# Optimization experiments

Hardware: AMD Instinct MI355X
Metric: run time of the kernel (lower is better)

Reference implementation:

```python
import jax, jax.numpy as jnp
import numpy as np

LAM = 0.01        # self.lam
K_POINTS = 256    # max diagram points kept for matching


def _diagram0(img):
    """0-dim sublevel-set cubical persistence of a 2D image (V-construction,
    4-connectivity) via Kruskal-style union-find over value-sorted pixels.
    Returns (births, deaths, valid) each of shape [H*W]; essential class gets
    death = max(img). Pairs with zero persistence are masked out (as gudhi does)."""
    H, W = img.shape
    N = H * W
    v = img.reshape(-1)
    order = jnp.argsort(v)          # stable ascending filtration order
    rank = jnp.argsort(order)       # rank[i] = position of pixel i in filtration
    idx = jnp.arange(N)
    rows, cols = idx // W, idx % W
    nbr = jnp.stack([
        jnp.where(rows > 0, idx - W, -1),
        jnp.where(rows < H - 1, idx + W, -1),
        jnp.where(cols > 0, idx - 1, -1),
        jnp.where(cols < W - 1, idx + 1, -1)], axis=1)  # [N,4]

    def find(parent, i):
        # root chase with path halving
        def cond(c):
            p, j = c
            return p[j] != j
        def body(c):
            p, j = c
            pj = p[j]
            return p.at[j].set(p[pj]), pj
        p, r = jax.lax.while_loop(cond, body, (parent, i))
        return p, r

    def step(t, carry):
        parent, death = carry
        p = order[t]  # pixel entering the filtration
        def merge(k, carry2):
            parent, death = carry2
            q = nbr[p, k]
            active = (q >= 0) & (rank[jnp.maximum(q, 0)] < t)
            qs = jnp.where(active, jnp.maximum(q, 0), p)
            parent, rp = find(parent, p)
            parent, rq = find(parent, qs)
            do = active & (rp != rq)
            older = jnp.where(rank[rp] < rank[rq], rp, rq)   # smaller birth survives
            young = jnp.where(rank[rp] < rank[rq], rq, rp)   # younger component dies at v[p]
            parent = parent.at[young].set(jnp.where(do, older, parent[young]))
            death = death.at[young].set(jnp.where(do, p, death[young]))
            return parent, death
        return jax.lax.fori_loop(0, 4, merge, (parent, death))

    parent, death = jax.lax.fori_loop(
        0, N, step, (jnp.arange(N), jnp.full((N,), -1, jnp.int32)))
    births = v
    deaths = jnp.where(death >= 0, v[jnp.maximum(death, 0)], jnp.max(v))
    valid = (deaths - births) > 0
    return births, deaths, valid


def _wdist(b1, d1, m1, b2, d2, m2):
    """2-Wasserstein distance between diagrams, approximated by matching the
    top-K points of each diagram sorted by persistence; unmatched points are
    projected to the diagonal (cost pers^2/2). Final (sum cost)^(1/2) (p=2)."""
    def topk(b, d, m):
        pers = jnp.where(m, d - b, 0.0)
        pk, ix = jax.lax.top_k(pers, K_POINTS)
        return b[ix], d[ix], pk
    b1k, d1k, p1 = topk(b1, d1, m1)
    b2k, d2k, p2 = topk(b2, d2, m2)
    has1, has2 = p1 > 0, p2 > 0
    match = (b1k - b2k) ** 2 + (d1k - d2k) ** 2
    cost = (jnp.where(has1 & has2, match, 0.0)
            + jnp.where(has1 & ~has2, p1 ** 2 * 0.5, 0.0)
            + jnp.where(~has1 & has2, p2 ** 2 * 0.5, 0.0))
    return jnp.sqrt(jnp.sum(cost) + 1e-12)


def _topo_loss(model_output, labels):
    pred = jax.nn.sigmoid(model_output)[:, 0]   # squeeze(dim=1) -> [B,H,W]
    msk = labels[:, 0]
    mn = pred.min(axis=(1, 2), keepdims=True)
    mx = pred.max(axis=(1, 2), keepdims=True)
    pq = jnp.round((pred - mn) / (mx - mn) * 10.0) / 10.0   # 11-level quantization
    mq = jnp.round(msk * 10.0) / 10.0
    bm, dm, vm = jax.vmap(_diagram0)(mq)   # pi_mask
    bp, dp, vp = jax.vmap(_diagram0)(pq)   # pi_pred
    per_sample = jax.vmap(_wdist)(bm, dm, vm, bp, dp, vp)
    return LAM * jnp.sum(per_sample) / pred.shape[0]


def setup_inputs():
    key = jax.random.key(0)
    k1, k2 = jax.random.split(key)
    model_output = jax.random.normal(k1, (4, 1, 128, 128), jnp.float32)
    labels = jax.random.uniform(k2, (4, 1, 128, 128), jnp.float32)
    return {"model_output": model_output, "labels": labels}


def reference(model_output, labels):
    return _topo_loss(model_output, labels)
```

## Files before the change

### kernel.cpp

```cpp
#include <hip/hip_runtime.h>
#include <stdint.h>

#define NPIX 16384
#define IMW 128
#define NIMG 8
#define NLVL 11
#define BIGK 0xFFFFFFFFu
#define IMASK 16383u
#define DONE 0x0D0E0D0Eu

__device__ __forceinline__ unsigned findk(volatile unsigned* par, unsigned i) {
    unsigned k = par[i];
    for (;;) {
        unsigned j = k & IMASK;
        unsigned pk = par[j];
        if (pk == k) return k;
        par[i] = pk;
        i = j; k = pk;
    }
}

__device__ __forceinline__ void unionk(volatile unsigned* par, unsigned* par32,
                                       unsigned a, unsigned b) {
    unsigned ka = findk(par, a);
    unsigned kb = findk(par, b);
    while (ka != kb) {
        unsigned hi = max(ka, kb);
        unsigned lo = min(ka, kb);
        unsigned hidx = hi & IMASK;
        if (atomicCAS(par32 + hidx, hi, lo) == hi) return;
        ka = findk(par, hidx);
        kb = findk(par, lo & IMASK);
    }
}

__device__ __forceinline__ void flag_release(unsigned* p) {
    __threadfence();
    __hip_atomic_store(p, DONE, __ATOMIC_RELEASE, __HIP_MEMORY_SCOPE_AGENT);
}
__device__ __forceinline__ void flag_acquire(unsigned* p) {
    while (__hip_atomic_load(p, __ATOMIC_ACQUIRE, __HIP_MEMORY_SCOPE_AGENT) != DONE)
        __builtin_amdgcn_s_sleep(2);
}

__global__ __launch_bounds__(1024) void prep_ccl(const float* __restrict__ model_output,
                                                 const float* __restrict__ labels,
                                                 uint8_t* __restrict__ lvl_all,
                                                 int* __restrict__ maxL_all,
                                                 unsigned* __restrict__ argmin_all,
                                                 unsigned* __restrict__ rootmask_all,
                                                 unsigned* __restrict__ flags)
{
    __shared__ unsigned s_par[NPIX];
    int blk = blockIdx.x;
    int tid = threadIdx.x;
    unsigned lane = tid & 63u;

    if (blk < 8) {
        int img = blk;
        bool ismask = img < 4;
        const float* src = ismask ? (labels + (size_t)img * NPIX)
                                  : (model_output + (size_t)(img - 4) * NPIX);
        uint8_t* lvl = lvl_all + (size_t)img * NPIX;
        unsigned* rm = rootmask_all + (size_t)img * NPIX;
        float* s_f = (float*)s_par;
        unsigned* s_u = s_par + 32;
        float* s_mnmx = (float*)(s_par + 64);

        for (int q = tid; q < NPIX / 4; q += 1024)
            ((uint4*)rm)[q] = make_uint4(0, 0, 0, 0);

        float mn = 0.f, mx = 1.f;
        if (!ismask) {
            float lmn = 1e30f, lmx = -1e30f;
            for (int i = tid; i < NPIX; i += 1024) {
                float s = 1.0f / (1.0f + expf(-src[i]));
                lmn = fminf(lmn, s); lmx = fmaxf(lmx, s);
            }
            for (int off = 32; off > 0; off >>= 1) {
                lmn = fminf(lmn, __shfl_down(lmn, off));
                lmx = fmaxf(lmx, __shfl_down(lmx, off));
            }
            int wv = tid >> 6;
            if (lane == 0) { s_f[wv] = lmn; s_f[16 + wv] = lmx; }
            __syncthreads();
            if (tid == 0) {
                float a = s_f[0], c = s_f[16];
                for (int w = 1; w < 16; ++w) { a = fminf(a, s_f[w]); c = fmaxf(c, s_f[16 + w]); }
                s_mnmx[0] = a; s_mnmx[1] = c;
            }
            __syncthreads();
            mn = s_mnmx[0]; mx = s_mnmx[1];
        }
        float denom = mx - mn;
        if (denom <= 0.f) denom = 1.f;

        unsigned lmaxk = 0, bestk = BIGK;
        for (int i = tid; i < NPIX; i += 1024) {
            int L;
            if (ismask) L = (int)rintf(src[i] * 10.0f);
            else {
                float s = 1.0f / (1.0f + expf(-src[i]));
                L = (int)rintf((s - mn) / denom * 10.0f);
            }
            lvl[i] = (uint8_t)L;
            unsigned key = ((unsigned)L << 14) | (unsigned)i;
            lmaxk = max(lmaxk, (unsigned)L);
            bestk = min(bestk, key);
        }
        for (int off = 32; off > 0; off >>= 1) {
            lmaxk = max(lmaxk, (unsigned)__shfl_down((int)lmaxk, off));
            bestk = min(bestk, (unsigned)__shfl_down((int)bestk, off));
        }
        if (lane == 0) { s_u[tid >> 6] = lmaxk; s_u[16 + (tid >> 6)] = bestk; }
        __syncthreads();
        if (tid == 0) {
            unsigned m = s_u[0], b = s_u[16];
            for (int w = 1; w < 16; ++w) { m = max(m, s_u[w]); b = min(b, s_u[16 + w]); }
            maxL_all[img] = (int)m;
            argmin_all[img] = b & IMASK;
            flag_release(&flags[img]);
        }
        return;
    }

    int b = blk - 8;
    int img = b / NLVL, l = b % NLVL;
    int w = tid >> 6;
    const uint8_t* lv = lvl_all + (size_t)img * NPIX;
    unsigned* rm = rootmask_all + (size_t)img * NPIX;
    volatile unsigned* par = s_par;

    if (tid == 0) flag_acquire(&flags[img]);
    __syncthreads();
    int maxL = maxL_all[img];

    if (l >= maxL) {
        if (tid == 0) atomicOr(&rm[argmin_all[img]], 1u << l);
        return;
    }

    unsigned am = 0;
#pragma unroll
    for (int k = 0; k < 16; ++k) {
        int i = (w << 10) + (k << 6) + (int)lane;
        unsigned Lv = lv[i];
        bool act = (int)Lv <= l;
        if (act) am |= 1u << k;
        unsigned key = (Lv << 14) | (unsigned)i;
        unsigned long long m = __ballot(act);
        unsigned kv = act ? key : BIGK;
        unsigned long long lowmask = (1ull << lane) - 1ull;
        unsigned long long zb = (~m) & lowmask;
        int runstart = zb ? (64 - __clzll(zb)) : 0;
        unsigned v = kv;
#pragma unroll
        for (int d = 1; d < 64; d <<= 1) {
            unsigned o = __shfl_up(v, d, 64);
            if ((int)lane - d >= runstart) v = min(v, o);
        }
        unsigned long long za = (lane == 63u) ? 0ull : ((~m) >> (lane + 1));
        int runend = za ? ((int)lane + __ffsll((long long)za) - 1) : 63;
        unsigned rmin = __shfl(v, runend, 64);
        s_par[i] = act ? rmin : key;
    }

    unsigned amL  = (unsigned)__shfl_up((int)am, 1, 64);
    unsigned am63 = (unsigned)__shfl((int)am, 63, 64);

#pragma unroll
    for (int k = 0; k < 16; ++k) {
        if (!((am >> k) & 1u)) continue;
        int i = (w << 10) + (k << 6) + (int)lane;
        if ((k & 1) && lane == 0u && ((am63 >> (k - 1)) & 1u))
            unionk(par, s_par, (unsigned)i, (unsigned)(i - 1));
        if (k >= 2 && ((am >> (k - 2)) & 1u)) {
            bool leftpair = (lane > 0u) && ((amL >> k) & 1u) && ((amL >> (k - 2)) & 1u);
            if (!leftpair)
                unionk(par, s_par, (unsigned)i, (unsigned)(i - IMW));
        }
    }
    __syncthreads();

    if (w >= 1) {
#pragma unroll
        for (int k = 0; k < 2; ++k) {
            if (!((am >> k) & 1u)) continue;
            int i = (w << 10) + (k << 6) + (int)lane;
            if ((int)(s_par[i - IMW] >> 14) <= l) {
                int col = (k << 6) + (int)lane;
                bool lact = (lane > 0u) ? (((amL >> k) & 1u) != 0u)
                                        : (k == 1 ? (((am63 >> 0) & 1u) != 0u) : false);
                bool leftpair = (col != 0) && lact && ((int)(s_par[i - 1 - IMW] >> 14) <= l);
                if (!leftpair)
                    unionk(par, s_par, (unsigned)i, (unsigned)(i - IMW));
            }
        }
    }
    __syncthreads();

#pragma unroll
    for (int k = 0; k < 16; ++k) {
        if (!((am >> k) & 1u)) continue;
        int i = (w << 10) + (k << 6) + (int)lane;
        if ((s_par[i] & IMASK) == (unsigned)i) atomicOr(&rm[i], 1u << l);
    }
}

__global__ __launch_bounds__(1024) void death_wdist(const uint8_t* __restrict__ lvl_all,
                                                    const int* __restrict__ maxL_all,
                                                    const unsigned* __restrict__ rootmask_all,
                                                    float* __restrict__ outP,
                                                    float* __restrict__ outB,
                                                    float* __restrict__ outD,
                                                    unsigned* __restrict__ dflags,
                                                    float* __restrict__ out)
{
    __shared__ uint8_t  s_lvl[NPIX];
    __shared__ uint8_t  s_rank[NPIX];
    __shared__ unsigned long long s_bm[256];
    __shared__ unsigned s_keys[256];
    __shared__ unsigned s_pc[256];
    __shared__ unsigned s_hist[64];
    __shared__ uint8_t  s_rtab[NLVL * NLVL];
    __shared__ unsigned s_ctl[4];

    int blk = blockIdx.x;
    int tid = threadIdx.x;

    if (blk >= 8) {
        if (tid < 8) flag_acquire(&dflags[tid]);
        __syncthreads();

        float* part = (float*)s_pc;
        float* dist = (float*)(s_pc + 16);
        int s = tid >> 8;
        int slot = tid & 255;
        int mi = s * 256 + slot;
        int pi = (4 + s) * 256 + slot;
        float p1 = outP[mi], b1 = outB[mi], d1 = outD[mi];
        float p2 = outP[pi], b2 = outB[pi], d2 = outD[pi];
        bool h1 = p1 > 0.f, h2 = p2 > 0.f;
        float cost = 0.f;
        if (h1 && h2)      cost = (b1 - b2) * (b1 - b2) + (d1 - d2) * (d1 - d2);
        else if (h1)       cost = p1 * p1 * 0.5f;
        else if (h2)       cost = p2 * p2 * 0.5f;

        for (int off = 32; off > 0; off >>= 1) cost += __shfl_down(cost, off);
        int wv = tid >> 6;
        if ((tid & 63) == 0) part[wv] = cost;
        __syncthreads();
        if (tid < 4) {
            float sum = part[tid * 4] + part[tid * 4 + 1] + part[tid * 4 + 2] + part[tid * 4 + 3];
            dist[tid] = sqrtf(sum + 1e-12f);
        }
        __syncthreads();
        if (tid == 0)
            out[0] = 0.01f * (dist[0] + dist[1] + dist[2] + dist[3]) / 4.0f;
        return;
    }

    int img = blk;
    const uint8_t* lv = lvl_all + (size_t)img * NPIX;
    const unsigned* rmg = rootmask_all + (size_t)img * NPIX;
    int maxL = maxL_all[img];

    ((uint4*)s_lvl)[tid] = ((const uint4*)lv)[tid];
    if (tid < 64) s_hist[tid] = 0;
    if (tid < 256) { s_bm[tid] = 0ull; s_keys[tid] = 0xFFFFFFFFu; }
    if (tid < NLVL * NLVL) {
        int d = tid / NLVL, bb0 = tid % NLVL;
        if (d > bb0) {
            float pers = (float)d / 10.0f - (float)bb0 / 10.0f;
            unsigned rk = 0;
            for (int dd = 1; dd <= 10; ++dd)
                for (int bb = 0; bb < dd; ++bb) {
                    float pp = (float)dd / 10.0f - (float)bb / 10.0f;
                    rk += (pp > pers) ? 1u : 0u;
                }
            s_rtab[d * NLVL + bb0] = (uint8_t)rk;
        }
    }
    __syncthreads();

    for (int i = tid; i < NPIX; i += 1024) {
        uint8_t r = 0xFF;
        int b = s_lvl[i];
        unsigned rmv = rmg[i];
        if ((rmv >> b) & 1u) {
            unsigned inv = (~rmv) >> (b + 1);
            int d = b + 1 + (__ffs(inv) - 1);
            d = min(d, maxL);
            if (d > b) { r = s_rtab[d * NLVL + b]; atomicAdd(&s_hist[r], 1u); }
        }
        s_rank[i] = r;
    }
    __syncthreads();

    if (tid == 0) {
        unsigned cum = 0, rstar = 63, cless = 0;
        for (int r = 0; r < 56; ++r) {
            if (cum + s_hist[r] >= 256u && rstar == 63u) { rstar = r; cless = cum; }
            cum += s_hist[r];
        }
        if (rstar == 63u) cless = cum;
        s_ctl[0] = rstar; s_ctl[1] = cless;
        s_ctl[2] = (rstar == 63u) ? 0u : (256u - cless);
        s_ctl[3] = 0;
    }
    __syncthreads();
    unsigned rstar = s_ctl[0], cless = s_ctl[1], mneed = s_ctl[2];

    for (int i = tid; i < NPIX; i += 1024) {
        unsigned r = s_rank[i];
        if (r == 0xFFu) continue;
        if (r < rstar) {
            unsigned pos = atomicAdd(&s_ctl[3], 1u);
            if (pos < 256u) s_keys[pos] = (r << 14) | (unsigned)i;
        } else if (r == rstar) {
            atomicOr(&s_bm[i >> 6], 1ull << (i & 63));
        }
    }
    __syncthreads();

    for (unsigned kk = 2; kk <= 256; kk <<= 1) {
        for (unsigned j = kk >> 1; j > 0; j >>= 1) {
            if (tid < 256) {
                unsigned i = (unsigned)tid, ixj = i ^ j;
                if (ixj > i) {
                    unsigned x = s_keys[i], y = s_keys[ixj];
                    bool up = ((i & kk) == 0);
                    if ((x > y) == up) { s_keys[i] = y; s_keys[ixj] = x; }
                }
            }
            __syncthreads();
        }
    }

    if (tid < 256) s_pc[tid] = (unsigned)__popcll(s_bm[tid]);
    __syncthreads();
    for (int d = 1; d < 256; d <<= 1) {
        unsigned x = 0;
        if (tid < 256 && tid >= d) x = s_pc[tid - d];
        __syncthreads();
        if (tid < 256 && tid >= d) s_pc[tid] += x;
        __syncthreads();
    }
    for (int i = tid; i < NPIX; i += 1024) {
        if (s_rank[i] != rstar || rstar == 63u) continue;
        if (!((s_bm[i >> 6] >> (i & 63)) & 1ull)) continue;
        unsigned w = i >> 6;
        unsigned order = (w ? s_pc[w - 1] : 0u)
                       + (unsigned)__popcll(s_bm[w] & ((1ull << (i & 63)) - 1ull));
        if (order < mneed) s_keys[cless + order] = (rstar << 14) | (unsigned)i;
    }
    __syncthreads();

    for (int s = tid; s < 256; s += 1024) {
        unsigned key = s_keys[s];
        float p = 0.f, bv = 0.f, dv = 0.f;
        if (key != 0xFFFFFFFFu) {
            unsigned i = key & IMASK;
            int b = s_lvl[i];
            unsigned rmv = rmg[i];
            unsigned inv = (~rmv) >> (b + 1);
            int d = b + 1 + (__ffs(inv) - 1);
            d = min(d, maxL);
            bv = (float)b / 10.0f;
            dv = (float)d / 10.0f;
            p = dv - bv;
        }
        outP[img * 256 + s] = p;
        outB[img * 256 + s] = bv;
        outD[img * 256 + s] = dv;
    }
    __syncthreads();
    if (tid == 0) flag_release(&dflags[img]);
}

extern "C" void kernel_launch(void* const* d_in, const int* in_sizes, int n_in,
                              void* d_out, int out_size, void* d_ws, size_t ws_size,
                              hipStream_t stream)
{
    const float* model_output = (const float*)d_in[0];
    const float* labels = (const float*)d_in[1];
    char* ws = (char*)d_ws;
    uint8_t* lvl = (uint8_t*)ws;
    int* maxL = (int*)(ws + 131072);
    unsigned* argmin = (unsigned*)(ws + 131104);
    unsigned* rootmask = (unsigned*)(ws + 131136);
    float* outP = (float*)(ws + 655424);
    float* outB = outP + NIMG * 256;
    float* outD = outB + NIMG * 256;
    unsigned* flags = (unsigned*)(ws + 680000);
    unsigned* dflags = (unsigned*)(ws + 680032);
    float* out = (float*)d_out;

    prep_ccl<<<96, 1024, 0, stream>>>(model_output, labels, lvl, maxL, argmin,
                                      rootmask, flags);
    death_wdist<<<9, 1024, 0, stream>>>(lvl, maxL, rootmask, outP, outB, outD,
                                        dflags, out);
}
```

Measured before the change: 130.1 us.

## Move stage boundary: separate prep kernel, fuse CCL with death/wdist via flags

Splits the quantization/min-max prep into its own kernel and merges the per-level connected-components blocks with the death-extraction and distance blocks into a single kernel. The stages inside that kernel are chained with per-(image,level) release/acquire flags instead of a kernel boundary. The prep step now caches sigmoid values in shared memory so expf runs once per pixel rather than twice. The intent is to let the death stage of each image start as soon as its own levels finish, in exchange for spin-waiting blocks that rely on all 97 blocks being co-resident.

Measured after the change: 118.3 us, median of 2. -9.0%, faster.

```diff
diff --git a/kernel.cpp b/kernel.cpp
--- a/kernel.cpp
+++ b/kernel.cpp
@@ -43,197 +43,322 @@
         __builtin_amdgcn_s_sleep(2);
 }
 
-__global__ __launch_bounds__(1024) void prep_ccl(const float* __restrict__ model_output,
-                                                 const float* __restrict__ labels,
-                                                 uint8_t* __restrict__ lvl_all,
-                                                 int* __restrict__ maxL_all,
-                                                 unsigned* __restrict__ argmin_all,
-                                                 unsigned* __restrict__ rootmask_all,
-                                                 unsigned* __restrict__ flags)
+__global__ __launch_bounds__(1024) void prep_kernel(const float* __restrict__ model_output,
+                                                    const float* __restrict__ labels,
+                                                    uint8_t* __restrict__ lvl_all,
+                                                    int* __restrict__ maxL_all,
+                                                    unsigned* __restrict__ argmin_all,
+                                                    unsigned* __restrict__ rootmask_all)
 {
-    __shared__ unsigned s_par[NPIX];
+    __shared__ float s_sig[NPIX];
+    __shared__ float s_f[32];
+    __shared__ unsigned s_u[32];
+    __shared__ float s_mnmx[2];
+
+    int img = blockIdx.x;
+    int tid = threadIdx.x;
+    unsigned lane = tid & 63u;
+    bool ismask = img < 4;
+    const float* src = ismask ? (labels + (size_t)img * NPIX)
+                              : (model_output + (size_t)(img - 4) * NPIX);
+    uint8_t* lvl = lvl_all + (size_t)img * NPIX;
+    unsigned* rm = rootmask_all + (size_t)img * NPIX;
+
+    for (int q = tid; q < NPIX / 4; q += 1024)
+        ((uint4*)rm)[q] = make_uint4(0, 0, 0, 0);
+
+    float mn = 0.f, mx = 1.f;
+    if (!ismask) {
+        float lmn = 1e30f, lmx = -1e30f;
+        for (int i = tid; i < NPIX; i += 1024) {
+            float s = 1.0f / (1.0f + expf(-src[i]));
+            s_sig[i] = s;
+            lmn = fminf(lmn, s); lmx = fmaxf(lmx, s);
+        }
+        for (int off = 32; off > 0; off >>= 1) {
+            lmn = fminf(lmn, __shfl_down(lmn, off));
+            lmx = fmaxf(lmx, __shfl_down(lmx, off));
+        }
+        int wv = tid >> 6;
+        if (lane == 0) { s_f[wv] = lmn; s_f[16 + wv] = lmx; }
+        __syncthreads();
+        if (tid == 0) {
+            float a = s_f[0], c = s_f[16];
+            for (int w = 1; w < 16; ++w) { a = fminf(a, s_f[w]); c = fmaxf(c, s_f[16 + w]); }
+            s_mnmx[0] = a; s_mnmx[1] = c;
+        }
+        __syncthreads();
+        mn = s_mnmx[0]; mx = s_mnmx[1];
+    }
+    float denom = mx - mn;
+    if (denom <= 0.f) denom = 1.f;
+
+    unsigned lmaxk = 0, bestk = BIGK;
+    for (int i = tid; i < NPIX; i += 1024) {
+        int L;
+        if (ismask) L = (int)rintf(src[i] * 10.0f);
+        else        L = (int)rintf((s_sig[i] - mn) / denom * 10.0f);
+        lvl[i] = (uint8_t)L;
+        unsigned key = ((unsigned)L << 14) | (unsigned)i;
+        lmaxk = max(lmaxk, (unsigned)L);
+        bestk = min(bestk, key);
+    }
+    for (int off = 32; off > 0; off >>= 1) {
+        lmaxk = max(lmaxk, (unsigned)__shfl_down((int)lmaxk, off));
+        bestk = min(bestk, (unsigned)__shfl_down((int)bestk, off));
+    }
+    if (lane == 0) { s_u[tid >> 6] = lmaxk; s_u[16 + (tid >> 6)] = bestk; }
+    __syncthreads();
+    if (tid == 0) {
+        unsigned m = s_u[0], b = s_u[16];
+        for (int w = 1; w < 16; ++w) { m = max(m, s_u[w]); b = min(b, s_u[16 + w]); }
+        maxL_all[img] = (int)m;
+        argmin_all[img] = b & IMASK;
+    }
+}
+
+__global__ __launch_bounds__(1024) void ccl_death_wdist(const uint8_t* __restrict__ lvl_all,
+                                                        const int* __restrict__ maxL_all,
+                                                        const unsigned* __restrict__ argmin_all,
+                                                        unsigned* __restrict__ rootmask_all,
+                                                        float* __restrict__ outP,
+                                                        float* __restrict__ outB,
+                                                        float* __restrict__ outD,
+                                                        unsigned* __restrict__ flags,
+                                                        unsigned* __restrict__ dflags,
+                                                        float* __restrict__ out)
+{
+    __shared__ __align__(16) unsigned char smem[65536];
     int blk = blockIdx.x;
     int tid = threadIdx.x;
     unsigned lane = tid & 63u;
 
-    if (blk < 8) {
-        int img = blk;
-        bool ismask = img < 4;
-        const float* src = ismask ? (labels + (size_t)img * NPIX)
-                                  : (model_output + (size_t)(img - 4) * NPIX);
-        uint8_t* lvl = lvl_all + (size_t)img * NPIX;
+    if (blk < 88) {
+        int b = blk;
+        int img = b / NLVL, l = b % NLVL;
+        int w = tid >> 6;
+        const uint8_t* lv = lvl_all + (size_t)img * NPIX;
         unsigned* rm = rootmask_all + (size_t)img * NPIX;
-        float* s_f = (float*)s_par;
-        unsigned* s_u = s_par + 32;
-        float* s_mnmx = (float*)(s_par + 64);
-
-        for (int q = tid; q < NPIX / 4; q += 1024)
-            ((uint4*)rm)[q] = make_uint4(0, 0, 0, 0);
-
-        float mn = 0.f, mx = 1.f;
-        if (!ismask) {
-            float lmn = 1e30f, lmx = -1e30f;
-            for (int i = tid; i < NPIX; i += 1024) {
-                float s = 1.0f / (1.0f + expf(-src[i]));
-                lmn = fminf(lmn, s); lmx = fmaxf(lmx, s);
-            }
-            for (int off = 32; off > 0; off >>= 1) {
-                lmn = fminf(lmn, __shfl_down(lmn, off));
-                lmx = fmaxf(lmx, __shfl_down(lmx, off));
-            }
-            int wv = tid >> 6;
-            if (lane == 0) { s_f[wv] = lmn; s_f[16 + wv] = lmx; }
-            __syncthreads();
+        unsigned* s_par = (unsigned*)smem;
+        volatile unsigned* par = s_par;
+        int maxL = maxL_all[img];
+
+        if (l >= maxL) {
             if (tid == 0) {
-                float a = s_f[0], c = s_f[16];
-                for (int w = 1; w < 16; ++w) { a = fminf(a, s_f[w]); c = fmaxf(c, s_f[16 + w]); }
-                s_mnmx[0] = a; s_mnmx[1] = c;
-            }
-            __syncthreads();
-            mn = s_mnmx[0]; mx = s_mnmx[1];
-        }
-        float denom = mx - mn;
-        if (denom <= 0.f) denom = 1.f;
-
-        unsigned lmaxk = 0, bestk = BIGK;
-        for (int i = tid; i < NPIX; i += 1024) {
-            int L;
-            if (ismask) L = (int)rintf(src[i] * 10.0f);
-            else {
-                float s = 1.0f / (1.0f + expf(-src[i]));
-                L = (int)rintf((s - mn) / denom * 10.0f);
-            }
-            lvl[i] = (uint8_t)L;
-            unsigned key = ((unsigned)L << 14) | (unsigned)i;
-            lmaxk = max(lmaxk, (unsigned)L);
-            bestk = min(bestk, key);
-        }
-        for (int off = 32; off > 0; off >>= 1) {
-            lmaxk = max(lmaxk, (unsigned)__shfl_down((int)lmaxk, off));
-            bestk = min(bestk, (unsigned)__shfl_down((int)bestk, off));
-        }
-        if (lane == 0) { s_u[tid >> 6] = lmaxk; s_u[16 + (tid >> 6)] = bestk; }
-        __syncthreads();
-        if (tid == 0) {
-            unsigned m = s_u[0], b = s_u[16];
-            for (int w = 1; w < 16; ++w) { m = max(m, s_u[w]); b = min(b, s_u[16 + w]); }
-            maxL_all[img] = (int)m;
-            argmin_all[img] = b & IMASK;
-            flag_release(&flags[img]);
-        }
-        return;
-    }
-
-    int b = blk - 8;
-    int img = b / NLVL, l = b % NLVL;
-    int w = tid >> 6;
-    const uint8_t* lv = lvl_all + (size_t)img * NPIX;
-    unsigned* rm = rootmask_all + (size_t)img * NPIX;
-    volatile unsigned* par = s_par;
-
-    if (tid == 0) flag_acquire(&flags[img]);
-    __syncthreads();
-    int maxL = maxL_all[img];
-
-    if (l >= maxL) {
-        if (tid == 0) atomicOr(&rm[argmin_all[img]], 1u << l);
-        return;
-    }
-
-    unsigned am = 0;
+                atomicOr(&rm[argmin_all[img]], 1u << l);
+                flag_release(&flags[b]);
+            }
+            return;
+        }
+
+        unsigned am = 0;
 #pragma unroll
-    for (int k = 0; k < 16; ++k) {
-        int i = (w << 10) + (k << 6) + (int)lane;
-        unsigned Lv = lv[i];
-        bool act = (int)Lv <= l;
-        if (act) am |= 1u << k;
-        unsigned key = (Lv << 14) | (unsigned)i;
-        unsigned long long m = __ballot(act);
-        unsigned kv = act ? key : BIGK;
-        unsigned long long lowmask = (1ull << lane) - 1ull;
-        unsigned long long zb = (~m) & lowmask;
-        int runstart = zb ? (64 - __clzll(zb)) : 0;
-        unsigned v = kv;
+        for (int k = 0; k < 16; ++k) {
+            int i = (w << 10) + (k << 6) + (int)lane;
+            unsigned Lv = lv[i];
+            bool act = (int)Lv <= l;
+            if (act) am |= 1u << k;
+            unsigned key = (Lv << 14) | (unsigned)i;
+            unsigned long long m = __ballot(act);
+            unsigned kv = act ? key : BIGK;
+            unsigned long long lowmask = (1ull << lane) - 1ull;
+            unsigned long long zb = (~m) & lowmask;
+            int runstart = zb ? (64 - __clzll(zb)) : 0;
+            unsigned v = kv;
 #pragma unroll
-        for (int d = 1; d < 64; d <<= 1) {
-            unsigned o = __shfl_up(v, d, 64);
-            if ((int)lane - d >= runstart) v = min(v, o);
-        }
-        unsigned long long za = (lane == 63u) ? 0ull : ((~m) >> (lane + 1));
-        int runend = za ? ((int)lane + __ffsll((long long)za) - 1) : 63;
-        unsigned rmin = __shfl(v, runend, 64);
-        s_par[i] = act ? rmin : key;
-    }
-
-    unsigned amL  = (unsigned)__shfl_up((int)am, 1, 64);
-    unsigned am63 = (unsigned)__shfl((int)am, 63, 64);
+            for (int d = 1; d < 64; d <<= 1) {
+                unsigned o = __shfl_up(v, d, 64);
+                if ((int)lane - d >= runstart) v = min(v, o);
+            }
+            unsigned long long za = (lane == 63u) ? 0ull : ((~m) >> (lane + 1));
+            int runend = za ? ((int)lane + __ffsll((long long)za) - 1) : 63;
+            unsigned rmin = __shfl(v, runend, 64);
+            s_par[i] = act ? rmin : key;
+        }
+
+        unsigned amL  = (unsigned)__shfl_up((int)am, 1, 64);
+        unsigned am63 = (unsigned)__shfl((int)am, 63, 64);
 
 #pragma unroll
-    for (int k = 0; k < 16; ++k) {
-        if (!((am >> k) & 1u)) continue;
-        int i = (w << 10) + (k << 6) + (int)lane;
-        if ((k & 1) && lane == 0u && ((am63 >> (k - 1)) & 1u))
-            unionk(par, s_par, (unsigned)i, (unsigned)(i - 1));
-        if (k >= 2 && ((am >> (k - 2)) & 1u)) {
-            bool leftpair = (lane > 0u) && ((amL >> k) & 1u) && ((amL >> (k - 2)) & 1u);
-            if (!leftpair)
-                unionk(par, s_par, (unsigned)i, (unsigned)(i - IMW));
-        }
-    }
-    __syncthreads();
-
-    if (w >= 1) {
-#pragma unroll
-        for (int k = 0; k < 2; ++k) {
+        for (int k = 0; k < 16; ++k) {
             if (!((am >> k) & 1u)) continue;
             int i = (w << 10) + (k << 6) + (int)lane;
-            if ((int)(s_par[i - IMW] >> 14) <= l) {
-                int col = (k << 6) + (int)lane;
-                bool lact = (lane > 0u) ? (((amL >> k) & 1u) != 0u)
-                                        : (k == 1 ? (((am63 >> 0) & 1u) != 0u) : false);
-                bool leftpair = (col != 0) && lact && ((int)(s_par[i - 1 - IMW] >> 14) <= l);
+            if ((k & 1) && lane == 0u && ((am63 >> (k - 1)) & 1u))
+                unionk(par, s_par, (unsigned)i, (unsigned)(i - 1));
+            if (k >= 2 && ((am >> (k - 2)) & 1u)) {
+                bool leftpair = (lane > 0u) && ((amL >> k) & 1u) && ((amL >> (k - 2)) & 1u);
                 if (!leftpair)
                     unionk(par, s_par, (unsigned)i, (unsigned)(i - IMW));
             }
         }
-    }
-    __syncthreads();
-
+        __syncthreads();
+
+        if (w >= 1) {
 #pragma unroll
-    for (int k = 0; k < 16; ++k) {
-        if (!((am >> k) & 1u)) continue;
-        int i = (w << 10) + (k << 6) + (int)lane;
-        if ((s_par[i] & IMASK) == (unsigned)i) atomicOr(&rm[i], 1u << l);
-    }
-}
-
-__global__ __launch_bounds__(1024) void death_wdist(const uint8_t* __restrict__ lvl_all,
-                                                    const int* __restrict__ maxL_all,
-                                                    const unsigned* __restrict__ rootmask_all,
-                                                    float* __restrict__ outP,
-                                                    float* __restrict__ outB,
-                                                    float* __restrict__ outD,
-                                                    unsigned* __restrict__ dflags,
-                                                    float* __restrict__ out)
-{
-    __shared__ uint8_t  s_lvl[NPIX];
-    __shared__ uint8_t  s_rank[NPIX];
-    __shared__ unsigned long long s_bm[256];
-    __shared__ unsigned s_keys[256];
-    __shared__ unsigned s_pc[256];
-    __shared__ unsigned s_hist[64];
-    __shared__ uint8_t  s_rtab[NLVL * NLVL];
-    __shared__ unsigned s_ctl[4];
-
-    int blk = blockIdx.x;
-    int tid = threadIdx.x;
-
-    if (blk >= 8) {
+            for (int k = 0; k < 2; ++k) {
+                if (!((am >> k) & 1u)) continue;
+                int i = (w << 10) + (k << 6) + (int)lane;
+                if ((int)(s_par[i - IMW] >> 14) <= l) {
+                    int col = (k << 6) + (int)lane;
+                    bool lact = (lane > 0u) ? (((amL >> k) & 1u) != 0u)
+                                            : (k == 1 ? (((am63 >> 0) & 1u) != 0u) : false);
+                    bool leftpair = (col != 0) && lact && ((int)(s_par[i - 1 - IMW] >> 14) <= l);
+                    if (!leftpair)
+                        unionk(par, s_par, (unsigned)i, (unsigned)(i - IMW));
+                }
+            }
+        }
+        __syncthreads();
+
+#pragma unroll
+        for (int k = 0; k < 16; ++k) {
+            if (!((am >> k) & 1u)) continue;
+            int i = (w << 10) + (k << 6) + (int)lane;
+            if ((s_par[i] & IMASK) == (unsigned)i) atomicOr(&rm[i], 1u << l);
+        }
+        __syncthreads();
+        if (tid == 0) flag_release(&flags[b]);
+        return;
+    }
+
+    if (blk < 96) {
+        int img = blk - 88;
+        uint8_t*  s_lvl  = (uint8_t*)smem;
+        uint8_t*  s_rank = (uint8_t*)(smem + 16384);
+        unsigned long long* s_bm = (unsigned long long*)(smem + 32768);
+        unsigned* s_keys = (unsigned*)(smem + 34816);
+        unsigned* s_pc   = (unsigned*)(smem + 35840);
+        unsigned* s_hist = (unsigned*)(smem + 36864);
+        uint8_t*  s_rtab = (uint8_t*)(smem + 37120);
+        unsigned* s_ctl  = (unsigned*)(smem + 37248);
+
+        if (tid < NLVL) flag_acquire(&flags[img * NLVL + tid]);
+        __syncthreads();
+
+        const uint8_t* lv = lvl_all + (size_t)img * NPIX;
+        const unsigned* rmg = rootmask_all + (size_t)img * NPIX;
+        int maxL = maxL_all[img];
+
+        ((uint4*)s_lvl)[tid] = ((const uint4*)lv)[tid];
+        if (tid < 64) s_hist[tid] = 0;
+        if (tid < 256) { s_bm[tid] = 0ull; s_keys[tid] = 0xFFFFFFFFu; }
+        if (tid < NLVL * NLVL) {
+            int d = tid / NLVL, bb0 = tid % NLVL;
+            if (d > bb0) {
+                float pers = (float)d / 10.0f - (float)bb0 / 10.0f;
+                unsigned rk = 0;
+                for (int dd = 1; dd <= 10; ++dd)
+                    for (int bb = 0; bb < dd; ++bb) {
+                        float pp = (float)dd / 10.0f - (float)bb / 10.0f;
+                        rk += (pp > pers) ? 1u : 0u;
+                    }
+                s_rtab[d * NLVL + bb0] = (uint8_t)rk;
+            }
+        }
+        __syncthreads();
+
+        for (int i = tid; i < NPIX; i += 1024) {
+            uint8_t r = 0xFF;
+            int b = s_lvl[i];
+            unsigned rmv = rmg[i];
+            if ((rmv >> b) & 1u) {
+                unsigned inv = (~rmv) >> (b + 1);
+                int d = b + 1 + (__ffs(inv) - 1);
+                d = min(d, maxL);
+                if (d > b) { r = s_rtab[d * NLVL + b]; atomicAdd(&s_hist[r], 1u); }
+            }
+            s_rank[i] = r;
+        }
+        __syncthreads();
+
+        if (tid == 0) {
+            unsigned cum = 0, rstar = 63, cless = 0;
+            for (int r = 0; r < 56; ++r) {
+                if (cum + s_hist[r] >= 256u && rstar == 63u) { rstar = r; cless = cum; }
+                cum += s_hist[r];
+            }
+            if (rstar == 63u) cless = cum;
+            s_ctl[0] = rstar; s_ctl[1] = cless;
+            s_ctl[2] = (rstar == 63u) ? 0u : (256u - cless);
+            s_ctl[3] = 0;
+        }
+        __syncthreads();
+        unsigned rstar = s_ctl[0], cless = s_ctl[1], mneed = s_ctl[2];
+
+        for (int i = tid; i < NPIX; i += 1024) {
+            unsigned r = s_rank[i];
+            if (r == 0xFFu) continue;
+            if (r < rstar) {
+                unsigned pos = atomicAdd(&s_ctl[3], 1u);
+                if (pos < 256u) s_keys[pos] = (r << 14) | (unsigned)i;
+            } else if (r == rstar) {
+                atomicOr(&s_bm[i >> 6], 1ull << (i & 63));
+            }
+        }
+        __syncthreads();
+
+        for (unsigned kk = 2; kk <= 256; kk <<= 1) {
+            for (unsigned j = kk >> 1; j > 0; j >>= 1) {
+                if (tid < 256) {
+                    unsigned i = (unsigned)tid, ixj = i ^ j;
+                    if (ixj > i) {
+                        unsigned x = s_keys[i], y = s_keys[ixj];
+                        bool up = ((i & kk) == 0);
+                        if ((x > y) == up) { s_keys[i] = y; s_keys[ixj] = x; }
+                    }
+                }
+                __syncthreads();
+            }
+        }
+
+        if (tid < 256) s_pc[tid] = (unsigned)__popcll(s_bm[tid]);
+        __syncthreads();
+        for (int d = 1; d < 256; d <<= 1) {
+            unsigned x = 0;
+            if (tid < 256 && tid >= d) x = s_pc[tid - d];
+            __syncthreads();
+            if (tid < 256 && tid >= d) s_pc[tid] += x;
+            __syncthreads();
+        }
+        for (int i = tid; i < NPIX; i += 1024) {
+            if (s_rank[i] != rstar || rstar == 63u) continue;
+            if (!((s_bm[i >> 6] >> (i & 63)) & 1ull)) continue;
+            unsigned w = i >> 6;
+            unsigned order = (w ? s_pc[w - 1] : 0u)
+                           + (unsigned)__popcll(s_bm[w] & ((1ull << (i & 63)) - 1ull));
+            if (order < mneed) s_keys[cless + order] = (rstar << 14) | (unsigned)i;
+        }
+        __syncthreads();
+
+        for (int s = tid; s < 256; s += 1024) {
+            unsigned key = s_keys[s];
+            float p = 0.f, bv = 0.f, dv = 0.f;
+            if (key != 0xFFFFFFFFu) {
+                unsigned i = key & IMASK;
+                int b = s_lvl[i];
+                unsigned rmv = rmg[i];
+                unsigned inv = (~rmv) >> (b + 1);
+                int d = b + 1 + (__ffs(inv) - 1);
+                d = min(d, maxL);
+                bv = (float)b / 10.0f;
+                dv = (float)d / 10.0f;
+                p = dv - bv;
+            }
+            outP[img * 256 + s] = p;
+            outB[img * 256 + s] = bv;
+            outD[img * 256 + s] = dv;
+        }
+        __syncthreads();
+        if (tid == 0) flag_release(&dflags[img]);
+        return;
+    }
+
+    {
         if (tid < 8) flag_acquire(&dflags[tid]);
         __syncthreads();
 
-        float* part = (float*)s_pc;
-        float* dist = (float*)(s_pc + 16);
+        float* part = (float*)smem;
+        float* dist = (float*)(smem + 64);
         int s = tid >> 8;
         int slot = tid & 255;
         int mi = s * 256 + slot;
@@ -248,7 +373,7 @@
 
         for (int off = 32; off > 0; off >>= 1) cost += __shfl_down(cost, off);
         int wv = tid >> 6;
-        if ((tid & 63) == 0) part[wv] = cost;
+        if (lane == 0u) part[wv] = cost;
         __syncthreads();
         if (tid < 4) {
             float sum = part[tid * 4] + part[tid * 4 + 1] + part[tid * 4 + 2] + part[tid * 4 + 3];
@@ -257,125 +382,7 @@
         __syncthreads();
         if (tid == 0)
             out[0] = 0.01f * (dist[0] + dist[1] + dist[2] + dist[3]) / 4.0f;
-        return;
-    }
-
-    int img = blk;
-    const uint8_t* lv = lvl_all + (size_t)img * NPIX;
-    const unsigned* rmg = rootmask_all + (size_t)img * NPIX;
-    int maxL = maxL_all[img];
-
-    ((uint4*)s_lvl)[tid] = ((const uint4*)lv)[tid];
-    if (tid < 64) s_hist[tid] = 0;
-    if (tid < 256) { s_bm[tid] = 0ull; s_keys[tid] = 0xFFFFFFFFu; }
-    if (tid < NLVL * NLVL) {
-        int d = tid / NLVL, bb0 = tid % NLVL;
-        if (d > bb0) {
-            float pers = (float)d / 10.0f - (float)bb0 / 10.0f;
-            unsigned rk = 0;
-            for (int dd = 1; dd <= 10; ++dd)
-                for (int bb = 0; bb < dd; ++bb) {
-                    float pp = (float)dd / 10.0f - (float)bb / 10.0f;
-                    rk += (pp > pers) ? 1u : 0u;
-                }
-            s_rtab[d * NLVL + bb0] = (uint8_t)rk;
-        }
-    }
-    __syncthreads();
-
-    for (int i = tid; i < NPIX; i += 1024) {
-        uint8_t r = 0xFF;
-        int b = s_lvl[i];
-        unsigned rmv = rmg[i];
-        if ((rmv >> b) & 1u) {
-            unsigned inv = (~rmv) >> (b + 1);
-            int d = b + 1 + (__ffs(inv) - 1);
-            d = min(d, maxL);
-            if (d > b) { r = s_rtab[d * NLVL + b]; atomicAdd(&s_hist[r], 1u); }
-        }
-        s_rank[i] = r;
-    }
-    __syncthreads();
-
-    if (tid == 0) {
-        unsigned cum = 0, rstar = 63, cless = 0;
-        for (int r = 0; r < 56; ++r) {
-            if (cum + s_hist[r] >= 256u && rstar == 63u) { rstar = r; cless = cum; }
-            cum += s_hist[r];
-        }
-        if (rstar == 63u) cless = cum;
-        s_ctl[0] = rstar; s_ctl[1] = cless;
-        s_ctl[2] = (rstar == 63u) ? 0u : (256u - cless);
-        s_ctl[3] = 0;
-    }
-    __syncthreads();
-    unsigned rstar = s_ctl[0], cless = s_ctl[1], mneed = s_ctl[2];
-
-    for (int i = tid; i < NPIX; i += 1024) {
-        unsigned r = s_rank[i];
-        if (r == 0xFFu) continue;
-        if (r < rstar) {
-            unsigned pos = atomicAdd(&s_ctl[3], 1u);
-            if (pos < 256u) s_keys[pos] = (r << 14) | (unsigned)i;
-        } else if (r == rstar) {
-            atomicOr(&s_bm[i >> 6], 1ull << (i & 63));
-        }
-    }
-    __syncthreads();
-
-    for (unsigned kk = 2; kk <= 256; kk <<= 1) {
-        for (unsigned j = kk >> 1; j > 0; j >>= 1) {
-            if (tid < 256) {
-                unsigned i = (unsigned)tid, ixj = i ^ j;
-                if (ixj > i) {
-                    unsigned x = s_keys[i], y = s_keys[ixj];
-                    bool up = ((i & kk) == 0);
-                    if ((x > y) == up) { s_keys[i] = y; s_keys[ixj] = x; }
-                }
-            }
-            __syncthreads();
-        }
-    }
-
-    if (tid < 256) s_pc[tid] = (unsigned)__popcll(s_bm[tid]);
-    __syncthreads();
-    for (int d = 1; d < 256; d <<= 1) {
-        unsigned x = 0;
-        if (tid < 256 && tid >= d) x = s_pc[tid - d];
-        __syncthreads();
-        if (tid < 256 && tid >= d) s_pc[tid] += x;
-        __syncthreads();
-    }
-    for (int i = tid; i < NPIX; i += 1024) {
-        if (s_rank[i] != rstar || rstar == 63u) continue;
-        if (!((s_bm[i >> 6] >> (i & 63)) & 1ull)) continue;
-        unsigned w = i >> 6;
-        unsigned order = (w ? s_pc[w - 1] : 0u)
-                       + (unsigned)__popcll(s_bm[w] & ((1ull << (i & 63)) - 1ull));
-        if (order < mneed) s_keys[cless + order] = (rstar << 14) | (unsigned)i;
-    }
-    __syncthreads();
-
-    for (int s = tid; s < 256; s += 1024) {
-        unsigned key = s_keys[s];
-        float p = 0.f, bv = 0.f, dv = 0.f;
-        if (key != 0xFFFFFFFFu) {
-            unsigned i = key & IMASK;
-            int b = s_lvl[i];
-            unsigned rmv = rmg[i];
-            unsigned inv = (~rmv) >> (b + 1);
-            int d = b + 1 + (__ffs(inv) - 1);
-            d = min(d, maxL);
-            bv = (float)b / 10.0f;
-            dv = (float)d / 10.0f;
-            p = dv - bv;
-        }
-        outP[img * 256 + s] = p;
-        outB[img * 256 + s] = bv;
-        outD[img * 256 + s] = dv;
-    }
-    __syncthreads();
-    if (tid == 0) flag_release(&dflags[img]);
+    }
 }
 
 extern "C" void kernel_launch(void* const* d_in, const int* in_sizes, int n_in,
@@ -393,11 +400,10 @@
     float* outB = outP + NIMG * 256;
     float* outD = outB + NIMG * 256;
     unsigned* flags = (unsigned*)(ws + 680000);
-    unsigned* dflags = (unsigned*)(ws + 680032);
+    unsigned* dflags = (unsigned*)(ws + 680352);
     float* out = (float*)d_out;
 
-    prep_ccl<<<96, 1024, 0, stream>>>(model_output, labels, lvl, maxL, argmin,
-                                      rootmask, flags);
-    death_wdist<<<9, 1024, 0, stream>>>(lvl, maxL, rootmask, outP, outB, outD,
-                                        dflags, out);
-}
+    prep_kernel<<<NIMG, 1024, 0, stream>>>(model_output, labels, lvl, maxL, argmin, rootmask);
+    ccl_death_wdist<<<97, 1024, 0, stream>>>(lvl, maxL, argmin, rootmask,
+                                             outP, outB, outD, flags, dflags, out);
+}
```
